# Optimization experiments

Measured on AMD Instinct MI355X. Metric: run time of the kernel, lower is better.

The kernel has to match this reference:

```python
import jax, jax.numpy as jnp
import numpy as np

WS = 8          # window size
HEADS = 6
DIM = 192


def _rel_idx(ws):
    # index [q, k] -> flat relative-position index into table of size (2ws-1)^2
    pos = jnp.arange(ws * ws)
    ph, pw = pos // ws, pos % ws
    rel_h = ph[None, :] - ph[:, None] + ws - 1  # k_h - q_h + ws - 1
    rel_w = pw[None, :] - pw[:, None] + ws - 1
    return rel_h * (2 * ws - 1) + rel_w  # [ws*ws, ws*ws]


def setup_inputs() -> dict:
    key = jax.random.key(0)
    ks = jax.random.split(key, 4)
    x = jax.random.normal(ks[0], (4, DIM, 256, 256), jnp.float32)
    qkv_w = jax.random.normal(ks[1], (3 * DIM, DIM), jnp.float32) * 0.02  # 1x1 conv
    qkv_b = jnp.zeros((3 * DIM,), jnp.float32)
    out_w = jax.random.normal(ks[2], (DIM, DIM), jnp.float32) * 0.02      # 1x1 conv
    out_b = jnp.zeros((DIM,), jnp.float32)
    rpe_table = jax.random.normal(ks[3], (HEADS, (2 * WS - 1) ** 2), jnp.float32) * 0.001
    return {"x": x, "qkv_w": qkv_w, "qkv_b": qkv_b,
            "out_w": out_w, "out_b": out_b, "rpe_table": rpe_table}


def reference(x, qkv_w, qkv_b, out_w, out_b, rpe_table):
    B, C, H, W = x.shape
    ws, heads = WS, HEADS
    hd, wd = H // ws, W // ws          # H,W chosen divisible by ws -> pad is no-op
    c = C // heads                     # head dim
    n = ws * ws                        # tokens per window

    # 1x1 conv to qkv
    qkv = jnp.einsum('bchw,oc->bohw', x, qkv_w) + qkv_b[None, :, None, None]
    # feat_to_win: b (3 heads c) (hd ws) (wd ws) -> 3, (b hd wd), heads, n, c
    qkv = qkv.reshape(B, 3, heads, c, hd, ws, wd, ws)
    qkv = qkv.transpose(1, 0, 4, 6, 2, 5, 7, 3).reshape(3, B * hd * wd, heads, n, c)
    q, k, v = qkv[0], qkv[1], qkv[2]

    bias = rpe_table[:, _rel_idx(ws)]  # [heads, n, n]
    scale = c ** -0.5
    scores = jnp.einsum('whqc,whkc->whqk', q, k) * scale + bias[None]
    attn = jax.nn.softmax(scores, axis=-1)
    out = jnp.einsum('whqk,whkc->whqc', attn, v)

    # win_to_feat: (b hd wd) heads n c -> b (heads c) H W
    out = out.reshape(B, hd, wd, heads, ws, ws, c)
    out = out.transpose(0, 3, 6, 1, 4, 2, 5).reshape(B, C, H, W)

    out = jnp.einsum('bchw,oc->bohw', out, out_w) + out_b[None, :, None, None]
    return out
```

## Files before the change

kernel.cpp:

```cpp
#include <hip/hip_runtime.h>
#include <cstdint>
#include <cstddef>

typedef __attribute__((ext_vector_type(8))) short short8;
typedef __attribute__((ext_vector_type(4))) float floatx4;
typedef __attribute__((ext_vector_type(16))) float floatx16;

#define SEG 50331648ull

__device__ __forceinline__ unsigned short bf16rne(float f) {
  union { float f; unsigned int u; } c; c.f = f;
  unsigned int u = c.u;
  return (unsigned short)((u + 0x7fffu + ((u >> 16) & 1u)) >> 16);
}
__device__ __forceinline__ unsigned int packbf(float a, float b) {
  return (unsigned int)bf16rne(a) | ((unsigned int)bf16rne(b) << 16);
}
__device__ __forceinline__ unsigned int cvtpk(float lo, float hi) {
  unsigned int r;
  asm("v_cvt_pk_bf16_f32 %0, %1, %2" : "=v"(r) : "v"(lo), "v"(hi));
  return r;
}

__global__ __launch_bounds__(256) void w_prep(
    const float* __restrict__ wq, const float* __restrict__ qb,
    const float* __restrict__ ow,
    unsigned short* __restrict__ wqb, unsigned short* __restrict__ owb,
    float* __restrict__ qbs) {
  const float S = 0.17677669529663687f;
  int id = blockIdx.x * 256 + threadIdx.x;
  if (id < 55296) {
    float s = (id < 18432) ? S : 1.0f;
    ((unsigned int*)wqb)[id] = packbf(wq[2 * id] * s, wq[2 * id + 1] * s);
  } else if (id < 55296 + 18432) {
    int j = id - 55296;
    ((unsigned int*)owb)[j] = packbf(ow[2 * j], ow[2 * j + 1]);
  } else if (id < 55296 + 18432 + 576) {
    int j = id - 55296 - 18432;
    qbs[j] = qb[j] * (j < 192 ? S : 1.0f);
  }
}

__global__ void bias_prep(const float* __restrict__ rpe, float* __restrict__ bias_d) {
  const int head = blockIdx.x;
  const int tid = threadIdx.x;
  for (int e = tid; e < 4096; e += 256) {
    int f = e >> 10;
    int lane = (e >> 4) & 63;
    int reg = e & 15;
    int kt2 = f >> 1, qt2 = f & 1;
    int qq = qt2 * 32 + (lane & 31);
    int kk = kt2 * 32 + (reg & 3) + 8 * (reg >> 2) + 4 * (lane >> 5);
    int idx = ((kk >> 3) - (qq >> 3) + 7) * 15 + ((kk & 7) - (qq & 7) + 7);
    bias_d[((size_t)(head * 4 + f) * 64 + lane) * 16 + reg] = rpe[head * 225 + idx];
  }
}

#define WP 200
#define XP 200
__global__ __launch_bounds__(256) void qkv_mm(
    const float* __restrict__ x, const unsigned short* __restrict__ wqb,
    const float* __restrict__ qbs,
    unsigned short* __restrict__ q, unsigned short* __restrict__ k,
    unsigned short* __restrict__ v) {
  __shared__ unsigned short Xl[128 * XP];
  __shared__ union UB { unsigned short Wl[64 * WP]; float Tl[64][65]; } U;
  const int tid = threadIdx.x;
  const int pt = blockIdx.x, b = blockIdx.y;
  const int lane = tid & 63, w = tid >> 6;
  const int n16 = lane & 15, quad = lane >> 4;

  {
    const float* xbase = x + (size_t)b * 192 * 65536 + (size_t)pt * 128;
    const int row = tid >> 2, cb = (tid & 3) * 4;
    const int p_l = tid >> 2, c0 = (tid & 3) * 16;
#pragma unroll 1
    for (int tile = 0; tile < 6; ++tile) {
      int cc = tile >> 1, ph = tile & 1;
      const float* src = xbase + (size_t)(cc * 64 + row) * 65536 + ph * 64;
#pragma unroll
      for (int rr = 0; rr < 4; ++rr) {
        int col = cb + rr * 16;
        *(float4*)&U.Tl[row][col] = *(const float4*)(src + col);
      }
      __syncthreads();
      unsigned int wd[8];
#pragma unroll
      for (int e = 0; e < 8; ++e)
        wd[e] = cvtpk(U.Tl[c0 + 2 * e][p_l], U.Tl[c0 + 2 * e + 1][p_l]);
      unsigned short* xd = &Xl[(ph * 64 + p_l) * XP + cc * 64];
      *(uint4*)(xd + c0)     = make_uint4(wd[0], wd[1], wd[2], wd[3]);
      *(uint4*)(xd + c0 + 8) = make_uint4(wd[4], wd[5], wd[6], wd[7]);
      __syncthreads();
    }
  }

  int wrow[6], wcol[6];
#pragma unroll
  for (int r = 0; r < 6; ++r) {
    int id = tid + 256 * r;
    wrow[r] = id / 24;
    wcol[r] = (id - wrow[r] * 24) * 8;
  }
  short8 wpre[6];
#pragma unroll
  for (int r = 0; r < 6; ++r)
    wpre[r] = *(const short8*)(wqb + (size_t)wrow[r] * 192 + wcol[r]);
#pragma unroll
  for (int r = 0; r < 6; ++r)
    *(short8*)&U.Wl[wrow[r] * WP + wcol[r]] = wpre[r];
  __syncthreads();

  const floatx4 fz = {0.f, 0.f, 0.f, 0.f};
#pragma unroll 1
  for (int ot = 0; ot < 9; ++ot) {
    if (ot < 8) {
      const unsigned short* wn = wqb + (size_t)(ot + 1) * 64 * 192;
#pragma unroll
      for (int r = 0; r < 6; ++r)
        wpre[r] = *(const short8*)(wn + (size_t)wrow[r] * 192 + wcol[r]);
    }
    floatx4 acc[4][2];
#pragma unroll
    for (int i = 0; i < 4; ++i)
#pragma unroll
      for (int j = 0; j < 2; ++j) acc[i][j] = fz;
#pragma unroll
    for (int k0 = 0; k0 < 192; k0 += 32) {
      short8 a[4], bf[2];
#pragma unroll
      for (int i = 0; i < 4; ++i)
        a[i] = *(const short8*)&U.Wl[(16 * i + n16) * WP + k0 + quad * 8];
#pragma unroll
      for (int j = 0; j < 2; ++j)
        bf[j] = *(const short8*)&Xl[(w * 32 + 16 * j + n16) * XP + k0 + quad * 8];
#pragma unroll
      for (int i = 0; i < 4; ++i)
#pragma unroll
        for (int j = 0; j < 2; ++j)
          acc[i][j] = __builtin_amdgcn_mfma_f32_16x16x32_bf16(a[i], bf[j], acc[i][j], 0, 0, 0);
    }
    __syncthreads();
    if (ot < 8) {
#pragma unroll
      for (int r = 0; r < 6; ++r)
        *(short8*)&U.Wl[wrow[r] * WP + wcol[r]] = wpre[r];
    }
    __syncthreads();

    const int sel = ot / 3;
    unsigned short* dst = (sel == 0) ? q : ((sel == 1) ? k : v);
    const int h = pt >> 1;
#pragma unroll
    for (int j = 0; j < 2; ++j) {
      int wcol2 = w * 32 + 16 * j + n16;
      int wc = ((pt & 1) << 7) + wcol2;
      int win = (b << 10) + (h >> 3) * 32 + (wc >> 3);
      int t = ((h & 7) << 3) + (wc & 7);
#pragma unroll
      for (int i = 0; i < 4; ++i) {
        int og = ot * 64 + 16 * i + quad * 4;
        int off = og - sel * 192;
        int head = off >> 5, c = off & 31;
        float4 bb = *(const float4*)(qbs + og);
        float v0 = acc[i][j][0] + bb.x;
        float v1 = acc[i][j][1] + bb.y;
        float v2 = acc[i][j][2] + bb.z;
        float v3 = acc[i][j][3] + bb.w;
        *(uint2*)(dst + ((size_t)(win * 6 + head) * 64 + t) * 32 + c) =
            make_uint2(cvtpk(v0, v1), cvtpk(v2, v3));
      }
    }
  }
}

__global__ __launch_bounds__(256) void attn(
    const unsigned short* __restrict__ q, const unsigned short* __restrict__ k,
    const unsigned short* __restrict__ v, const float* __restrict__ bias_d,
    unsigned short* __restrict__ AO) {
  __shared__ unsigned short vl[4][32 * 72];
  const int tid = threadIdx.x, w = tid >> 6, lane = tid & 63;
  const int m32 = lane & 31, half = lane >> 5;
  const int wh = blockIdx.x * 4 + w;
  const int win = wh / 6, head = wh - win * 6;
  const unsigned short* qb = q + (size_t)wh * 2048;
  const unsigned short* kb = k + (size_t)wh * 2048;
  const unsigned short* vb = v + (size_t)wh * 2048;

  short8 vrow[4];
#pragma unroll
  for (int c8 = 0; c8 < 4; ++c8)
    vrow[c8] = *(const short8*)(vb + lane * 32 + c8 * 8);

  short8 ka[2][2];
#pragma unroll
  for (int kt2 = 0; kt2 < 2; ++kt2)
#pragma unroll
    for (int cc = 0; cc < 2; ++cc)
      ka[kt2][cc] = *(const short8*)(kb + (size_t)(kt2 * 32 + m32) * 32 + cc * 16 + half * 8);

  unsigned short* vlw = (unsigned short*)vl[w];
#pragma unroll
  for (int c8 = 0; c8 < 4; ++c8)
#pragma unroll
    for (int e = 0; e < 8; ++e)
      vlw[(c8 * 8 + e) * 72 + lane] = (unsigned short)vrow[c8][e];

  short8 va[4];
#pragma unroll
  for (int k16 = 0; k16 < 4; ++k16)
    va[k16] = *(const short8*)&vlw[m32 * 72 + k16 * 16 + half * 8];

  const float* bD = bias_d + (size_t)head * 4096;
  const floatx16 fz16 = {0.f,0.f,0.f,0.f,0.f,0.f,0.f,0.f,0.f,0.f,0.f,0.f,0.f,0.f,0.f,0.f};

#pragma unroll
  for (int qt2 = 0; qt2 < 2; ++qt2) {
    float4 bb[8];
#pragma unroll
    for (int g = 0; g < 4; ++g)
      bb[g] = *(const float4*)(bD + ((size_t)(qt2 * 64) + lane) * 16 + g * 4);
#pragma unroll
    for (int g = 0; g < 4; ++g)
      bb[4 + g] = *(const float4*)(bD + ((size_t)((2 + qt2) * 64) + lane) * 16 + g * 4);

    short8 qf0 = *(const short8*)(qb + (size_t)(qt2 * 32 + m32) * 32 + half * 8);
    short8 qf1 = *(const short8*)(qb + (size_t)(qt2 * 32 + m32) * 32 + 16 + half * 8);

    floatx16 st0 = __builtin_amdgcn_mfma_f32_32x32x16_bf16(ka[0][0], qf0, fz16, 0, 0, 0);
    st0 = __builtin_amdgcn_mfma_f32_32x32x16_bf16(ka[0][1], qf1, st0, 0, 0, 0);
    floatx16 st1 = __builtin_amdgcn_mfma_f32_32x32x16_bf16(ka[1][0], qf0, fz16, 0, 0, 0);
    st1 = __builtin_amdgcn_mfma_f32_32x32x16_bf16(ka[1][1], qf1, st1, 0, 0, 0);

    float x[32];
#pragma unroll
    for (int r = 0; r < 16; ++r) x[r]      = st0[r] + ((const float*)&bb[r >> 2])[r & 3];
#pragma unroll
    for (int r = 0; r < 16; ++r) x[16 + r] = st1[r] + ((const float*)&bb[4 + (r >> 2)])[r & 3];

    float mx = x[0];
#pragma unroll
    for (int r = 1; r < 32; ++r) mx = fmaxf(mx, x[r]);
    mx = fmaxf(mx, __shfl_xor(mx, 32));
    float s = 0.f;
#pragma unroll
    for (int r = 0; r < 32; ++r) { x[r] = __expf(x[r] - mx); s += x[r]; }
    s += __shfl_xor(s, 32);
    float iv = 1.0f / s;

    unsigned int u[16];
#pragma unroll
    for (int j = 0; j < 16; ++j) u[j] = cvtpk(x[2 * j], x[2 * j + 1]);

    floatx16 o = fz16;
#pragma unroll
    for (int k16 = 0; k16 < 4; ++k16) {
      int base = (k16 >> 1) * 8 + (k16 & 1) * 4;
      unsigned int a0 = u[base + 0], b0 = u[base + 2];
      unsigned int a1 = u[base + 1], b1 = u[base + 3];
      asm("v_permlane32_swap_b32 %0, %1" : "+v"(a0), "+v"(b0));
      asm("v_permlane32_swap_b32 %0, %1" : "+v"(a1), "+v"(b1));
      union { unsigned int wd[4]; short8 s8; } bw;
      bw.wd[0] = a0; bw.wd[1] = a1; bw.wd[2] = b0; bw.wd[3] = b1;
      o = __builtin_amdgcn_mfma_f32_32x32x16_bf16(va[k16], bw.s8, o, 0, 0, 0);
    }

    const int t = qt2 * 32 + m32;
    const int bimg = win >> 10, rem = win & 1023;
    const int h0 = (rem >> 5) << 3, w0 = (rem & 31) << 3;
    const size_t pix = ((size_t)bimg << 16) + (size_t)(h0 + (t >> 3)) * 256 + w0 + (t & 7);
    unsigned short* dstp = AO + pix * 192 + head * 32 + half * 4;
#pragma unroll
    for (int g = 0; g < 4; ++g) {
      float v0 = o[4 * g + 0] * iv, v1 = o[4 * g + 1] * iv;
      float v2 = o[4 * g + 2] * iv, v3 = o[4 * g + 3] * iv;
      *(uint2*)(dstp + g * 8) = make_uint2(cvtpk(v0, v1), cvtpk(v2, v3));
    }
  }
}

__global__ __launch_bounds__(256) void out_mm(
    const unsigned short* __restrict__ AO, const unsigned short* __restrict__ owb,
    const float* __restrict__ b2, float* __restrict__ out) {
  __shared__ unsigned short Xl[128 * XP];
  __shared__ unsigned short Wl[64 * WP];
  const int tid = threadIdx.x;
  const int pt = blockIdx.x, b = blockIdx.y;
  const int lane = tid & 63, w = tid >> 6;
  const int n16 = lane & 15, quad = lane >> 4;

  const unsigned short* arow = AO + ((size_t)b * 65536 + (size_t)pt * 128) * 192;
#pragma unroll
  for (int r = 0; r < 12; ++r) {
    int c = tid + 256 * r;
    int row = c / 24;
    int col = (c - row * 24) * 8;
    short8 xv = *(const short8*)(arow + (size_t)c * 8);
    *(short8*)&Xl[row * XP + col] = xv;
  }
  int wrow[6], wcol[6];
#pragma unroll
  for (int r = 0; r < 6; ++r) {
    int id = tid + 256 * r;
    wrow[r] = id / 24;
    wcol[r] = (id - wrow[r] * 24) * 8;
  }
  short8 wpre[6];
#pragma unroll
  for (int r = 0; r < 6; ++r)
    wpre[r] = *(const short8*)(owb + (size_t)wrow[r] * 192 + wcol[r]);
#pragma unroll
  for (int r = 0; r < 6; ++r)
    *(short8*)&Wl[wrow[r] * WP + wcol[r]] = wpre[r];
  __syncthreads();

  const floatx4 fz = {0.f, 0.f, 0.f, 0.f};
#pragma unroll 1
  for (int ot = 0; ot < 3; ++ot) {
    if (ot < 2) {
      const unsigned short* wn = owb + (size_t)(ot + 1) * 64 * 192;
#pragma unroll
      for (int r = 0; r < 6; ++r)
        wpre[r] = *(const short8*)(wn + (size_t)wrow[r] * 192 + wcol[r]);
    }
    floatx4 acc[2][4];
#pragma unroll
    for (int i = 0; i < 2; ++i)
#pragma unroll
      for (int j = 0; j < 4; ++j) acc[i][j] = fz;
#pragma unroll
    for (int k0 = 0; k0 < 192; k0 += 32) {
      short8 a[2], bf[4];
#pragma unroll
      for (int i = 0; i < 2; ++i)
        a[i] = *(const short8*)&Xl[(w * 32 + 16 * i + n16) * XP + k0 + quad * 8];
#pragma unroll
      for (int j = 0; j < 4; ++j)
        bf[j] = *(const short8*)&Wl[(16 * j + n16) * WP + k0 + quad * 8];
#pragma unroll
      for (int i = 0; i < 2; ++i)
#pragma unroll
        for (int j = 0; j < 4; ++j)
          acc[i][j] = __builtin_amdgcn_mfma_f32_16x16x32_bf16(a[i], bf[j], acc[i][j], 0, 0, 0);
    }
    __syncthreads();
    if (ot < 2) {
#pragma unroll
      for (int r = 0; r < 6; ++r)
        *(short8*)&Wl[wrow[r] * WP + wcol[r]] = wpre[r];
    }
    __syncthreads();

#pragma unroll
    for (int j = 0; j < 4; ++j) {
      int o = ot * 64 + 16 * j + n16;
      float bj = b2[o];
      float* obase = out + ((size_t)b * 192 + o) * 65536 + (size_t)pt * 128;
#pragma unroll
      for (int i = 0; i < 2; ++i) {
        int p = w * 32 + 16 * i + quad * 4;
        *(float4*)(obase + p) = make_float4(acc[i][j][0] + bj, acc[i][j][1] + bj,
                                            acc[i][j][2] + bj, acc[i][j][3] + bj);
      }
    }
  }
}

extern "C" void kernel_launch(void* const* d_in, const int* in_sizes, int n_in,
                              void* d_out, int out_size, void* d_ws, size_t ws_size,
                              hipStream_t stream) {
  const float* x     = (const float*)d_in[0];
  const float* qkv_w = (const float*)d_in[1];
  const float* qkv_b = (const float*)d_in[2];
  const float* out_w = (const float*)d_in[3];
  const float* out_b = (const float*)d_in[4];
  const float* rpe   = (const float*)d_in[5];
  float* out = (float*)d_out;

  unsigned short* wqb = (unsigned short*)d_ws;
  unsigned short* owb = wqb + 110592;
  float* qbs = (float*)(owb + 36864);
  unsigned short* q  = (unsigned short*)d_ws + SEG;
  unsigned short* k  = q + SEG;
  unsigned short* v  = k + SEG;
  unsigned short* AO = v + SEG;
  float* bias_d = (float*)(AO + SEG);

  w_prep<<<291, 256, 0, stream>>>(qkv_w, qkv_b, out_w, wqb, owb, qbs);
  bias_prep<<<6, 256, 0, stream>>>(rpe, bias_d);
  qkv_mm<<<dim3(512, 4), 256, 0, stream>>>(x, wqb, qbs, q, k, v);
  attn<<<6144, 256, 0, stream>>>(q, k, v, bias_d, AO);
  out_mm<<<dim3(512, 4), 256, 0, stream>>>(AO, owb, out_b, out);
}
```

Before: 648.0 us.

## Split x fp32-to-bf16 transpose into separate kernel before QKV matmul

Moves the fp32 NCHW to bf16 pixel-major conversion of x out of qkv_mm into a standalone x_to_bf16 kernel. qkv_mm then loads contiguous bf16 rows directly into shared memory, dropping the per-block transpose loop and its syncs and shrinking LDS use. AO is aliased onto the xb buffer and the bias loads are hoisted out of the store loop. The cost is an extra kernel launch plus a full bf16 write and re-read of x through global memory.

After: 645.9 us. No clear change (-0.3%).

```diff
diff --git a/kernel.cpp b/kernel.cpp
--- a/kernel.cpp
+++ b/kernel.cpp
@@ -56,45 +56,59 @@
   }
 }
 
+__global__ __launch_bounds__(256) void x_to_bf16(const float* __restrict__ x,
+                                                 unsigned short* __restrict__ xb) {
+  __shared__ float Tl[64][65];
+  const int tid = threadIdx.x;
+  const int ptile = blockIdx.x, cc = blockIdx.y, b = blockIdx.z;
+  const float* src = x + ((size_t)(b * 192 + cc * 64)) * 65536 + ptile * 64;
+  {
+    int row = tid >> 2;
+    int cb = (tid & 3) * 4;
+#pragma unroll
+    for (int rr = 0; rr < 4; ++rr) {
+      int col = cb + rr * 16;
+      float4 v = *(const float4*)(src + (size_t)row * 65536 + col);
+      *(float4*)&Tl[row][col] = v;
+    }
+  }
+  __syncthreads();
+  unsigned short* dst = xb + ((size_t)b * 65536 + (size_t)ptile * 64) * 192 + cc * 64;
+  {
+    int p_l = tid >> 2;
+    int c0 = (tid & 3) * 16;
+    unsigned int w[8];
+#pragma unroll
+    for (int e = 0; e < 8; ++e)
+      w[e] = cvtpk(Tl[c0 + 2 * e][p_l], Tl[c0 + 2 * e + 1][p_l]);
+    *(uint4*)(dst + (size_t)p_l * 192 + c0)     = make_uint4(w[0], w[1], w[2], w[3]);
+    *(uint4*)(dst + (size_t)p_l * 192 + c0 + 8) = make_uint4(w[4], w[5], w[6], w[7]);
+  }
+}
+
 #define WP 200
 #define XP 200
 __global__ __launch_bounds__(256) void qkv_mm(
-    const float* __restrict__ x, const unsigned short* __restrict__ wqb,
+    const unsigned short* __restrict__ xb, const unsigned short* __restrict__ wqb,
     const float* __restrict__ qbs,
     unsigned short* __restrict__ q, unsigned short* __restrict__ k,
     unsigned short* __restrict__ v) {
   __shared__ unsigned short Xl[128 * XP];
-  __shared__ union UB { unsigned short Wl[64 * WP]; float Tl[64][65]; } U;
+  __shared__ unsigned short Wl[64 * WP];
   const int tid = threadIdx.x;
   const int pt = blockIdx.x, b = blockIdx.y;
   const int lane = tid & 63, w = tid >> 6;
   const int n16 = lane & 15, quad = lane >> 4;
 
-  {
-    const float* xbase = x + (size_t)b * 192 * 65536 + (size_t)pt * 128;
-    const int row = tid >> 2, cb = (tid & 3) * 4;
-    const int p_l = tid >> 2, c0 = (tid & 3) * 16;
-#pragma unroll 1
-    for (int tile = 0; tile < 6; ++tile) {
-      int cc = tile >> 1, ph = tile & 1;
-      const float* src = xbase + (size_t)(cc * 64 + row) * 65536 + ph * 64;
-#pragma unroll
-      for (int rr = 0; rr < 4; ++rr) {
-        int col = cb + rr * 16;
-        *(float4*)&U.Tl[row][col] = *(const float4*)(src + col);
-      }
-      __syncthreads();
-      unsigned int wd[8];
-#pragma unroll
-      for (int e = 0; e < 8; ++e)
-        wd[e] = cvtpk(U.Tl[c0 + 2 * e][p_l], U.Tl[c0 + 2 * e + 1][p_l]);
-      unsigned short* xd = &Xl[(ph * 64 + p_l) * XP + cc * 64];
-      *(uint4*)(xd + c0)     = make_uint4(wd[0], wd[1], wd[2], wd[3]);
-      *(uint4*)(xd + c0 + 8) = make_uint4(wd[4], wd[5], wd[6], wd[7]);
-      __syncthreads();
-    }
-  }
-
+  const unsigned short* xrow = xb + ((size_t)b * 65536 + (size_t)pt * 128) * 192;
+#pragma unroll
+  for (int r = 0; r < 12; ++r) {
+    int c = tid + 256 * r;
+    int row = c / 24;
+    int col = (c - row * 24) * 8;
+    short8 xv = *(const short8*)(xrow + (size_t)c * 8);
+    *(short8*)&Xl[row * XP + col] = xv;
+  }
   int wrow[6], wcol[6];
 #pragma unroll
   for (int r = 0; r < 6; ++r) {
@@ -108,7 +122,7 @@
     wpre[r] = *(const short8*)(wqb + (size_t)wrow[r] * 192 + wcol[r]);
 #pragma unroll
   for (int r = 0; r < 6; ++r)
-    *(short8*)&U.Wl[wrow[r] * WP + wcol[r]] = wpre[r];
+    *(short8*)&Wl[wrow[r] * WP + wcol[r]] = wpre[r];
   __syncthreads();
 
   const floatx4 fz = {0.f, 0.f, 0.f, 0.f};
@@ -130,7 +144,7 @@
       short8 a[4], bf[2];
 #pragma unroll
       for (int i = 0; i < 4; ++i)
-        a[i] = *(const short8*)&U.Wl[(16 * i + n16) * WP + k0 + quad * 8];
+        a[i] = *(const short8*)&Wl[(16 * i + n16) * WP + k0 + quad * 8];
 #pragma unroll
       for (int j = 0; j < 2; ++j)
         bf[j] = *(const short8*)&Xl[(w * 32 + 16 * j + n16) * XP + k0 + quad * 8];
@@ -144,13 +158,17 @@
     if (ot < 8) {
 #pragma unroll
       for (int r = 0; r < 6; ++r)
-        *(short8*)&U.Wl[wrow[r] * WP + wcol[r]] = wpre[r];
+        *(short8*)&Wl[wrow[r] * WP + wcol[r]] = wpre[r];
     }
     __syncthreads();
 
     const int sel = ot / 3;
     unsigned short* dst = (sel == 0) ? q : ((sel == 1) ? k : v);
     const int h = pt >> 1;
+    float4 bb[4];
+#pragma unroll
+    for (int i = 0; i < 4; ++i)
+      bb[i] = *(const float4*)(qbs + ot * 64 + 16 * i + quad * 4);
 #pragma unroll
     for (int j = 0; j < 2; ++j) {
       int wcol2 = w * 32 + 16 * j + n16;
@@ -162,13 +180,9 @@
         int og = ot * 64 + 16 * i + quad * 4;
         int off = og - sel * 192;
         int head = off >> 5, c = off & 31;
-        float4 bb = *(const float4*)(qbs + og);
-        float v0 = acc[i][j][0] + bb.x;
-        float v1 = acc[i][j][1] + bb.y;
-        float v2 = acc[i][j][2] + bb.z;
-        float v3 = acc[i][j][3] + bb.w;
         *(uint2*)(dst + ((size_t)(win * 6 + head) * 64 + t) * 32 + c) =
-            make_uint2(cvtpk(v0, v1), cvtpk(v2, v3));
+            make_uint2(cvtpk(acc[i][j][0] + bb[i].x, acc[i][j][1] + bb[i].y),
+                       cvtpk(acc[i][j][2] + bb[i].z, acc[i][j][3] + bb[i].w));
       }
     }
   }
@@ -377,18 +391,20 @@
   const float* rpe   = (const float*)d_in[5];
   float* out = (float*)d_out;
 
-  unsigned short* wqb = (unsigned short*)d_ws;
+  unsigned short* xb = (unsigned short*)d_ws;
+  unsigned short* AO = xb;
+  unsigned short* q  = xb + SEG;
+  unsigned short* k  = q + SEG;
+  unsigned short* v  = k + SEG;
+  unsigned short* wqb = v + SEG;
   unsigned short* owb = wqb + 110592;
   float* qbs = (float*)(owb + 36864);
-  unsigned short* q  = (unsigned short*)d_ws + SEG;
-  unsigned short* k  = q + SEG;
-  unsigned short* v  = k + SEG;
-  unsigned short* AO = v + SEG;
-  float* bias_d = (float*)(AO + SEG);
+  float* bias_d = qbs + 576;
 
   w_prep<<<291, 256, 0, stream>>>(qkv_w, qkv_b, out_w, wqb, owb, qbs);
   bias_prep<<<6, 256, 0, stream>>>(rpe, bias_d);
-  qkv_mm<<<dim3(512, 4), 256, 0, stream>>>(x, wqb, qbs, q, k, v);
+  x_to_bf16<<<dim3(1024, 3, 4), 256, 0, stream>>>(x, xb);
+  qkv_mm<<<dim3(512, 4), 256, 0, stream>>>(xb, wqb, qbs, q, k, v);
   attn<<<6144, 256, 0, stream>>>(q, k, v, bias_d, AO);
   out_mm<<<dim3(512, 4), 256, 0, stream>>>(AO, owb, out_b, out);
 }
```
